# Kernel optimization log

Hardware: AMD Instinct MI355X
Metric: run time of the kernel (lower is better)

Reference implementation:

```python
import jax, jax.numpy as jnp
import numpy as np

N_IN, N_OUT, BATCH, LEVELS = 8192, 256, 1024, 2


def binarize(x):
    # clip + sign with straight-through gradient (Ioffe trick)
    c = jnp.clip(x, -1.0, 1.0)
    return c + jax.lax.stop_gradient(jnp.sign(c) - c)


def setup_inputs() -> dict:
    key = jax.random.key(0)
    ks = jax.random.split(key, 5)
    stdv = 1.0 / np.sqrt(N_IN)
    x = jax.random.normal(ks[0], (LEVELS, BATCH, N_IN), dtype=jnp.float32)
    w = jax.random.normal(ks[1], (32, N_IN, N_OUT), dtype=jnp.float32) * stdv
    gamma = jnp.ones((1,), dtype=jnp.float32)
    rand_map_0 = jax.random.randint(ks[2], (N_IN,), 0, N_IN, dtype=jnp.int32)
    rand_map_1 = jax.random.randint(ks[3], (N_IN,), 0, N_IN, dtype=jnp.int32)
    rand_map_2 = jax.random.randint(ks[4], (N_IN,), 0, N_IN, dtype=jnp.int32)
    pruning_mask = jnp.ones((N_IN, N_OUT), dtype=jnp.float32)
    return {"x": x, "w": w, "gamma": gamma, "pruning_mask": pruning_mask,
            "rand_map_0": rand_map_0, "rand_map_1": rand_map_1, "rand_map_2": rand_map_2}


def reference(x, w, gamma, pruning_mask, rand_map_0, rand_map_1, rand_map_2):
    # levels==2, LUT==True, BINARY==True path of binary_dense
    constraint_gamma = jnp.abs(gamma[0])
    cw = constraint_gamma * binarize(w)            # [32, n_in, n_out]
    mw = cw * pruning_mask[None, :, :]             # pruned clamped weights
    B, n_out = x.shape[1], mw.shape[2]
    out = jnp.zeros((B, n_out), dtype=x.dtype)
    for l in range(LEVELS):
        xl = x[l]                                   # [B, n_in] residual-binarization level l
        # original input + three random-map gathered shuffles
        streams = [xl, xl[:, rand_map_0], xl[:, rand_map_1], xl[:, rand_map_2]]
        # pos = (1+sign)/2*|x|, neg = (1-sign)/2*|x|  (one-hot sign selectors scaled by magnitude)
        pos = [(1.0 + binarize(s)) * 0.5 * jnp.abs(s) for s in streams]
        neg = [(1.0 - binarize(s)) * 0.5 * jnp.abs(s) for s in streams]
        for c in range(16):                         # truth table over 4 binary inputs
            bits = [(c >> (3 - i)) & 1 for i in range(4)]  # x is MSB, xs2 is LSB; 0->pos, 1->neg
            f = pos[0] if bits[0] == 0 else neg[0]
            for i in range(1, 4):
                f = f * (pos[i] if bits[i] == 0 else neg[i])
            out = out + f @ mw[16 * l + c]
    return out
```

## Files before the change

### kernel.cpp

```cpp
#include <hip/hip_runtime.h>
#include <hip/hip_fp16.h>


#define N_IN   8192
#define N_OUT  256
#define BATCH  1024
#define LEVELS 2

#define KSLICES 64
#define BTILES  4
#define BT      256
#define CHUNK_K 8
#define ROWP    264

__global__ __launch_bounds__(256) void pass_mc(const float* __restrict__ x,
                                               const int* __restrict__ rm0,
                                               const int* __restrict__ rm1,
                                               const int* __restrict__ rm2,
                                               unsigned int* __restrict__ mc) {
  __shared__ float xrow[N_IN];
  const int lb = blockIdx.x;
  const size_t base = (size_t)lb * N_IN;
  const float4* xv = (const float4*)(x + base);
  const int t = threadIdx.x;
#pragma unroll
  for (int j = 0; j < 8; ++j) {
    float4 v = xv[t + j * 256];
    *(float4*)&xrow[4 * (t + j * 256)] = v;
  }
  __syncthreads();
#pragma unroll 4
  for (int j = 0; j < 32; ++j) {
    const int k = t + j * 256;
    const int r0 = rm0[k], r1 = rm1[k], r2 = rm2[k];
    const float s0 = xrow[k], s1 = xrow[r0], s2 = xrow[r1], s3 = xrow[r2];
    const float m = fabsf(s0 * s1 * s2 * s3);
    const unsigned c = ((s0 < 0.f) ? 8u : 0u) | ((s1 < 0.f) ? 4u : 0u) |
                       ((s2 < 0.f) ? 2u : 0u) | ((s3 < 0.f) ? 1u : 0u);
    mc[base + k] = (__float_as_uint(m) & ~0xFu) | c;
  }
}

__global__ __launch_bounds__(512, 2) void main_fma(const float* __restrict__ w,
                                                   const float* __restrict__ mask,
                                                   const unsigned int* __restrict__ mc,
                                                   float* __restrict__ part) {
  __shared__ __half lw[4 * 16 * ROWP];
  __shared__ unsigned int lmc[LEVELS * CHUNK_K * 256];

  const int ks = blockIdx.x;
  const int bt = blockIdx.y;
  const int t = threadIdx.x;
  const int lane = t & 63;
  const int wid = t >> 6;
  const int wb = wid * 32;

  float acc[32][4];
#pragma unroll
  for (int i = 0; i < 32; ++i) {
    acc[i][0] = 0.f; acc[i][1] = 0.f; acc[i][2] = 0.f; acc[i][3] = 0.f;
  }

  const int s_ku = t >> 7;
  const int s_r  = (t >> 3) & 15;
  const int s_ob = (t & 7) * 32;

  for (int kc = 0; kc < 128 / CHUNK_K; ++kc) {
    const int k0 = ks * 128 + kc * CHUNK_K;
    __syncthreads();
    {
      const int l = t >> 8, b = t & 255;
      const unsigned int* src =
          mc + ((size_t)(l * BATCH + bt * BT + b) * N_IN + k0);
      const uint4 v0 = *(const uint4*)src;
      const uint4 v1 = *(const uint4*)(src + 4);
      unsigned int* dst = &lmc[l * (CHUNK_K * 256) + b];
      dst[0 * 256] = v0.x; dst[1 * 256] = v0.y; dst[2 * 256] = v0.z; dst[3 * 256] = v0.w;
      dst[4 * 256] = v1.x; dst[5 * 256] = v1.y; dst[6 * 256] = v1.z; dst[7 * 256] = v1.w;
    }
    __syncthreads();

    for (int sub = 0; sub < 4; ++sub) {
      if (sub) __syncthreads();
      {
        const int u = sub * 4 + s_ku;
        const int l = u >> 3, kk = u & 7;
        const int k = k0 + kk;
        const int row = l * 16 + s_r;
        const float* wsrc = w + ((size_t)(row * N_IN + k) * N_OUT + s_ob);
        const float* msrc = mask + ((size_t)k * N_OUT + s_ob);
        __half hbuf[32];
#pragma unroll
        for (int j = 0; j < 8; ++j) {
          const float4 wv = *(const float4*)(wsrc + j * 4);
          const float4 mv = *(const float4*)(msrc + j * 4);
          hbuf[4 * j + 0] = __float2half((wv.x > 0.f) ? mv.x : ((wv.x < 0.f) ? -mv.x : 0.f));
          hbuf[4 * j + 1] = __float2half((wv.y > 0.f) ? mv.y : ((wv.y < 0.f) ? -mv.y : 0.f));
          hbuf[4 * j + 2] = __float2half((wv.z > 0.f) ? mv.z : ((wv.z < 0.f) ? -mv.z : 0.f));
          hbuf[4 * j + 3] = __float2half((wv.w > 0.f) ? mv.w : ((wv.w < 0.f) ? -mv.w : 0.f));
        }
        __half* dst = &lw[s_ku * (16 * ROWP) + s_r * ROWP + s_ob];
#pragma unroll
        for (int j = 0; j < 4; ++j) *(uint4*)(dst + j * 8) = *(const uint4*)&hbuf[j * 8];
      }
      __syncthreads();

#pragma unroll
      for (int ul = 0; ul < 4; ++ul) {
        const int u = sub * 4 + ul;
        const int l = u >> 3, kk = u & 7;
        const unsigned int* mrow = &lmc[l * (CHUNK_K * 256) + kk * 256 + wb];
        const __half* wbase = &lw[ul * (16 * ROWP)];
#pragma unroll
        for (int i = 0; i < 32; i += 4) {
          const uint4 q = *(const uint4*)(mrow + i);
#define DO_B(UQ, AI)                                                        \
  {                                                                         \
    const unsigned uq = (UQ);                                               \
    const float m = __uint_as_float(uq & ~0xFu);                            \
    union { uint2 u2; __half2 h[2]; } wv_;                                  \
    wv_.u2 = *(const uint2*)(wbase + (uq & 0xFu) * ROWP + lane * 4);        \
    acc[AI][0] += m * __half2float(wv_.h[0].x);                             \
    acc[AI][1] += m * __half2float(wv_.h[0].y);                             \
    acc[AI][2] += m * __half2float(wv_.h[1].x);                             \
    acc[AI][3] += m * __half2float(wv_.h[1].y);                             \
  }
          DO_B(q.x, i + 0)
          DO_B(q.y, i + 1)
          DO_B(q.z, i + 2)
          DO_B(q.w, i + 3)
#undef DO_B
        }
      }
    }
  }

  float* dst = part + ((size_t)(ks * BATCH + bt * BT + wb) * N_OUT) + lane * 4;
#pragma unroll
  for (int i = 0; i < 32; ++i) *(float4*)(dst + (size_t)i * N_OUT) = *(const float4*)acc[i];
}

__global__ __launch_bounds__(256) void reduce_part(const float* __restrict__ part,
                                                   const float* __restrict__ gamma,
                                                   float* __restrict__ out) {
  const int b = blockIdx.x, o = threadIdx.x;
  const float g = fabsf(gamma[0]);
  const float* p = part + (size_t)b * N_OUT + o;
  float s = 0.f;
#pragma unroll
  for (int ks = 0; ks < KSLICES; ++ks) s += p[(size_t)ks * BATCH * N_OUT];
  out[b * N_OUT + o] = g * s;
}

extern "C" void kernel_launch(void* const* d_in, const int* in_sizes, int n_in,
                              void* d_out, int out_size, void* d_ws, size_t ws_size,
                              hipStream_t stream) {
  const float* x     = (const float*)d_in[0];
  const float* w     = (const float*)d_in[1];
  const float* gamma = (const float*)d_in[2];
  const float* mask  = (const float*)d_in[3];
  const int* rm0     = (const int*)d_in[4];
  const int* rm1     = (const int*)d_in[5];
  const int* rm2     = (const int*)d_in[6];
  float* out = (float*)d_out;

  unsigned int* mc = (unsigned int*)d_ws;
  float* part = (float*)((char*)d_ws + (size_t)LEVELS * BATCH * N_IN * 4);
  (void)in_sizes; (void)n_in; (void)out_size; (void)ws_size;

  pass_mc<<<dim3(LEVELS * BATCH), 256, 0, stream>>>(x, rm0, rm1, rm2, mc);
  main_fma<<<dim3(KSLICES, BTILES), 512, 0, stream>>>(w, mask, mc, part);
  reduce_part<<<dim3(BATCH), 256, 0, stream>>>(part, gamma, out);
}
```

Baseline: 1.019 ms.

## Double-buffer weight tiles with register prefetch and remap block order

Weight loads for the next sub-step are issued into registers before the FMA phase, and the converted half-precision weight tile goes into a double-buffered LDS array. This lets the per-sub barrier be dropped and global latency overlap with compute. The grid becomes 1D with a remapped block index that spreads k-slices and batch tiles across XCDs/CUs, and the occupancy hint of 2 blocks is removed. The cost is more LDS and registers, which may lower occupancy.

```diff
diff --git a/kernel.cpp b/kernel.cpp
--- a/kernel.cpp
+++ b/kernel.cpp
@@ -41,15 +41,18 @@
   }
 }
 
-__global__ __launch_bounds__(512, 2) void main_fma(const float* __restrict__ w,
-                                                   const float* __restrict__ mask,
-                                                   const unsigned int* __restrict__ mc,
-                                                   float* __restrict__ part) {
-  __shared__ __half lw[4 * 16 * ROWP];
-  __shared__ unsigned int lmc[LEVELS * CHUNK_K * 256];
+__global__ __launch_bounds__(512) void main_fma(const float* __restrict__ w,
+                                                const float* __restrict__ mask,
+                                                const unsigned int* __restrict__ mc,
+                                                float* __restrict__ part) {
+  __shared__ __half lw[2][4 * 16 * ROWP];
+  __shared__ unsigned int lmc[LEVELS * CHUNK_K * BT];
 
-  const int ks = blockIdx.x;
-  const int bt = blockIdx.y;
+  const int bid = blockIdx.x;
+  const int wk = (bid & 7) * (KSLICES * BTILES / 8) + (bid >> 3);
+  const int ks = wk >> 2;
+  const int bt = wk & 3;
+
   const int t = threadIdx.x;
   const int lane = t & 63;
   const int wid = t >> 6;
@@ -65,6 +68,21 @@
   const int s_r  = (t >> 3) & 15;
   const int s_ob = (t & 7) * 32;
 
+  float4 wpre[8];
+  auto issue_prefetch = [&](int g) {
+    const int sub2 = g & 3;
+    const int k0p = ks * 128 + (g >> 2) * CHUNK_K;
+    const int u = sub2 * 4 + s_ku;
+    const int l = u >> 3, kk = u & 7;
+    const int kp = k0p + kk;
+    const int row = l * 16 + s_r;
+    const float* wsrc = w + ((size_t)(row * N_IN + kp) * N_OUT + s_ob);
+#pragma unroll
+    for (int j = 0; j < 8; ++j) wpre[j] = *(const float4*)(wsrc + j * 4);
+  };
+
+  issue_prefetch(0);
+
   for (int kc = 0; kc < 128 / CHUNK_K; ++kc) {
     const int k0 = ks * 128 + kc * CHUNK_K;
     __syncthreads();
@@ -74,43 +92,43 @@
           mc + ((size_t)(l * BATCH + bt * BT + b) * N_IN + k0);
       const uint4 v0 = *(const uint4*)src;
       const uint4 v1 = *(const uint4*)(src + 4);
-      unsigned int* dst = &lmc[l * (CHUNK_K * 256) + b];
-      dst[0 * 256] = v0.x; dst[1 * 256] = v0.y; dst[2 * 256] = v0.z; dst[3 * 256] = v0.w;
-      dst[4 * 256] = v1.x; dst[5 * 256] = v1.y; dst[6 * 256] = v1.z; dst[7 * 256] = v1.w;
+      unsigned int* dst = &lmc[l * (CHUNK_K * BT) + b];
+      dst[0 * BT] = v0.x; dst[1 * BT] = v0.y; dst[2 * BT] = v0.z; dst[3 * BT] = v0.w;
+      dst[4 * BT] = v1.x; dst[5 * BT] = v1.y; dst[6 * BT] = v1.z; dst[7 * BT] = v1.w;
     }
     __syncthreads();
 
     for (int sub = 0; sub < 4; ++sub) {
-      if (sub) __syncthreads();
+      const int g = kc * 4 + sub;
+      const int buf = g & 1;
       {
         const int u = sub * 4 + s_ku;
         const int l = u >> 3, kk = u & 7;
         const int k = k0 + kk;
-        const int row = l * 16 + s_r;
-        const float* wsrc = w + ((size_t)(row * N_IN + k) * N_OUT + s_ob);
         const float* msrc = mask + ((size_t)k * N_OUT + s_ob);
         __half hbuf[32];
 #pragma unroll
         for (int j = 0; j < 8; ++j) {
-          const float4 wv = *(const float4*)(wsrc + j * 4);
+          const float4 wv = wpre[j];
           const float4 mv = *(const float4*)(msrc + j * 4);
           hbuf[4 * j + 0] = __float2half((wv.x > 0.f) ? mv.x : ((wv.x < 0.f) ? -mv.x : 0.f));
           hbuf[4 * j + 1] = __float2half((wv.y > 0.f) ? mv.y : ((wv.y < 0.f) ? -mv.y : 0.f));
           hbuf[4 * j + 2] = __float2half((wv.z > 0.f) ? mv.z : ((wv.z < 0.f) ? -mv.z : 0.f));
           hbuf[4 * j + 3] = __float2half((wv.w > 0.f) ? mv.w : ((wv.w < 0.f) ? -mv.w : 0.f));
         }
-        __half* dst = &lw[s_ku * (16 * ROWP) + s_r * ROWP + s_ob];
+        __half* dst = &lw[buf][s_ku * (16 * ROWP) + s_r * ROWP + s_ob];
 #pragma unroll
         for (int j = 0; j < 4; ++j) *(uint4*)(dst + j * 8) = *(const uint4*)&hbuf[j * 8];
       }
+      if (g + 1 < 64) issue_prefetch(g + 1);
       __syncthreads();
 
 #pragma unroll
       for (int ul = 0; ul < 4; ++ul) {
         const int u = sub * 4 + ul;
         const int l = u >> 3, kk = u & 7;
-        const unsigned int* mrow = &lmc[l * (CHUNK_K * 256) + kk * 256 + wb];
-        const __half* wbase = &lw[ul * (16 * ROWP)];
+        const unsigned int* mrow = &lmc[l * (CHUNK_K * BT) + kk * BT + wb];
+        const __half* wbase = &lw[buf][ul * (16 * ROWP)];
 #pragma unroll
         for (int i = 0; i < 32; i += 4) {
           const uint4 q = *(const uint4*)(mrow + i);
@@ -169,6 +187,6 @@
   (void)in_sizes; (void)n_in; (void)out_size; (void)ws_size;
 
   pass_mc<<<dim3(LEVELS * BATCH), 256, 0, stream>>>(x, rm0, rm1, rm2, mc);
-  main_fma<<<dim3(KSLICES, BTILES), 512, 0, stream>>>(w, mask, mc, part);
+  main_fma<<<dim3(KSLICES * BTILES), 512, 0, stream>>>(w, mask, mc, part);
   reduce_part<<<dim3(BATCH), 256, 0, stream>>>(part, gamma, out);
 }
```

After: 914.2 us. 1.11x faster.
